# Kernel tuning notes

Measured on AMD Instinct MI355X. Metric: run time of the kernel, lower is better.

Reference implementation:

```python
import jax, jax.numpy as jnp
import numpy as np

NUM_HEADS = 16

def setup_inputs() -> dict:
    key = jax.random.key(0)
    k1, k2, k3 = jax.random.split(key, 3)
    B, N, D = 4, 2048, 1024
    init_attn_std = D ** (-0.5)
    x = jax.random.normal(k1, (B, N, D), dtype=jnp.float32)
    qkv_w = jax.random.normal(k2, (D, 3 * D), dtype=jnp.float32) * init_attn_std
    proj_w = jax.random.normal(k3, (D, D), dtype=jnp.float32) * init_attn_std
    proj_b = jnp.zeros((D,), dtype=jnp.float32)
    return {"x": x, "qkv_w": qkv_w, "proj_w": proj_w, "proj_b": proj_b}

def reference(x, qkv_w, proj_w, proj_b):
    B, N, D = x.shape
    H = NUM_HEADS
    hd = D // H
    scale = hd ** (-0.5)
    # QKV projection (no bias, qkv_bias=False)
    qkv = (x @ qkv_w).reshape(B, N, 3, H, hd)
    q, k, v = jnp.moveaxis(qkv, 2, 0)  # each [B, N, H, hd]
    # scaled dot-product attention with causal mask (matches flax nn.dot_product_attention)
    scores = jnp.einsum('bqhd,bkhd->bhqk', q * scale, k)  # [B, H, N, N]
    causal = jnp.tril(jnp.ones((N, N), dtype=bool))
    big_neg = jnp.finfo(scores.dtype).min
    scores = jnp.where(causal, scores, big_neg)
    attn = jax.nn.softmax(scores, axis=-1)
    out = jnp.einsum('bhqk,bkhd->bqhd', attn, v).reshape(B, N, D)
    # output projection (proj_bias=True)
    return out @ proj_w + proj_b
```

## Files before the change

### kernel.cpp

```cpp
#include <hip/hip_runtime.h>

typedef __attribute__((ext_vector_type(8))) short sh8;
typedef __attribute__((ext_vector_type(8))) __bf16 bf8v;
typedef __attribute__((ext_vector_type(4))) float f4v;
typedef __attribute__((ext_vector_type(16))) float f16v;
typedef __attribute__((ext_vector_type(4))) unsigned u4v;

__device__ __forceinline__ float fast_exp2(float x) { return __builtin_amdgcn_exp2f(x); }

__device__ __forceinline__ unsigned short f2bf(float f) {
  unsigned u = __builtin_bit_cast(unsigned, f);
  u += 0x7fffu + ((u >> 16) & 1u);
  return (unsigned short)(u >> 16);
}
__device__ __forceinline__ float bf2f(unsigned short h) {
  unsigned u = ((unsigned)h) << 16;
  return __builtin_bit_cast(float, u);
}

__device__ __forceinline__ void glds16(const unsigned short* g, unsigned short* l) {
  __builtin_amdgcn_global_load_lds((const __attribute__((address_space(1))) void*)g,
                                   (__attribute__((address_space(3))) void*)l, 16, 0, 0);
}

__global__ __launch_bounds__(256) void cast_kernel(const float* __restrict__ in,
                                                   unsigned short* __restrict__ out) {
  const int idx = (blockIdx.x * 256 + threadIdx.x) * 4;
  const float4 v = *(const float4*)(in + idx);
  ushort4 o;
  o.x = f2bf(v.x); o.y = f2bf(v.y); o.z = f2bf(v.z); o.w = f2bf(v.w);
  *(ushort4*)(out + idx) = o;
}

__global__ __launch_bounds__(256) void transpose_cast_kernel(const float* __restrict__ in,
                                                             unsigned short* __restrict__ out,
                                                             int R, int C) {
  __shared__ float tile[32][33];
  const int c0 = blockIdx.x * 32, r0 = blockIdx.y * 32;
  const int tx = threadIdx.x, ty = threadIdx.y;
#pragma unroll
  for (int i = 0; i < 4; ++i)
    tile[ty + 8 * i][tx] = in[(size_t)(r0 + ty + 8 * i) * C + c0 + tx];
  __syncthreads();
#pragma unroll
  for (int i = 0; i < 4; ++i)
    out[(size_t)(c0 + ty + 8 * i) * R + r0 + tx] = f2bf(tile[tx][ty + 8 * i]);
}

__global__ __launch_bounds__(256) void transpose_v_kernel(
    const unsigned short* __restrict__ V, unsigned short* __restrict__ Vt) {
  __shared__ alignas(16) unsigned short T[64 * 64];
  const int bh = blockIdx.y;
  const int n0 = blockIdx.x * 64;
  const int tid = threadIdx.x;
  {
    const int r = tid >> 2;
    const int seg = tid & 3;
#pragma unroll
    for (int s = 0; s < 2; ++s) {
      const int sg = seg + 4 * s;
      const sh8 v = *(const sh8*)&V[((size_t)bh * 2048 + n0 + r) * 64 + sg * 8];
      *(sh8*)&T[r * 64 + ((sg * 8) ^ ((r & 7) << 3))] = v;
    }
  }
  __syncthreads();
  const int d = tid & 63;
  const int h2 = tid >> 6;
  unsigned buf[8];
#pragma unroll
  for (int t = 0; t < 8; ++t) {
    const int n1 = h2 * 16 + 2 * t;
    const unsigned short a = T[n1 * 64 + (d ^ ((n1 & 7) << 3))];
    const unsigned short b = T[(n1 + 1) * 64 + (d ^ (((n1 + 1) & 7) << 3))];
    buf[t] = (unsigned)a | ((unsigned)b << 16);
  }
  unsigned short* dst = Vt + ((size_t)bh * 64 + d) * 2048 + n0 + h2 * 16;
  *(uint4*)dst = *(uint4*)&buf[0];
  *(uint4*)(dst + 8) = *(uint4*)&buf[4];
}

template <int MODE>
__global__ __launch_bounds__(256) void gemm_bf16_kernel(
    const unsigned short* __restrict__ A,
    const unsigned short* __restrict__ Bt,
    int M, int N, int K,
    unsigned short* __restrict__ q_out, unsigned short* __restrict__ k_out,
    unsigned short* __restrict__ v_out,
    const float* __restrict__ bias, float* __restrict__ c_out) {
  constexpr int BM = 128, BN = 128, BK = 32;
  __shared__ alignas(16) unsigned short As[BM * 32];
  __shared__ alignas(16) unsigned short Bs[BN * 32];
  const int tid = threadIdx.x;
  const int lane = tid & 63;
  const int wave = tid >> 6;
  const int wr = (wave >> 1) * 64;
  const int wc = (wave & 1) * 64;
  const int bm = blockIdx.x * BM;
  const int bn = blockIdx.y * BN;
  const int fr = lane & 15;
  const int kq = lane >> 4;

  f4v acc[4][4] = {};

  const int r16 = lane >> 2;
  const int slot = (lane & 3) ^ (r16 & 3);

  for (int k0 = 0; k0 < K; k0 += BK) {
    __syncthreads();
#pragma unroll
    for (int s = 0; s < 2; ++s) {
      const int rbase = wave * 32 + s * 16;
      glds16(&A[(size_t)(bm + rbase + r16) * K + k0 + slot * 8], &As[rbase * 32]);
      glds16(&Bt[(size_t)(bn + rbase + r16) * K + k0 + slot * 8], &Bs[rbase * 32]);
    }
    __syncthreads();
    bf8v af[4], bfv[4];
#pragma unroll
    for (int m = 0; m < 4; ++m) {
      const int row = wr + m * 16 + fr;
      af[m] = __builtin_bit_cast(bf8v, *(const sh8*)&As[row * 32 + ((kq * 8) ^ ((row & 3) << 3))]);
    }
#pragma unroll
    for (int n = 0; n < 4; ++n) {
      const int row = wc + n * 16 + fr;
      bfv[n] = __builtin_bit_cast(bf8v, *(const sh8*)&Bs[row * 32 + ((kq * 8) ^ ((row & 3) << 3))]);
    }
#pragma unroll
    for (int m = 0; m < 4; ++m)
#pragma unroll
      for (int n = 0; n < 4; ++n)
        acc[m][n] = __builtin_amdgcn_mfma_f32_16x16x32_bf16(af[m], bfv[n], acc[m][n], 0, 0, 0);
  }

#pragma unroll
  for (int m = 0; m < 4; ++m) {
#pragma unroll
    for (int n = 0; n < 4; ++n) {
#pragma unroll
      for (int i = 0; i < 4; ++i) {
        const int r = bm + wr + m * 16 + kq * 4 + i;
        const int c = bn + wc + n * 16 + fr;
        const float val = acc[m][n][i];
        if (MODE == 0) {
          const int b = r >> 11, nidx = r & 2047;
          const int which = c >> 10, rem = c & 1023;
          const int h = rem >> 6, d = rem & 63;
          const size_t off = ((size_t)((b * 16 + h) * 2048 + nidx)) * 64 + d;
          if (which == 0)      q_out[off] = f2bf(val * 0.18033688f);
          else if (which == 1) k_out[off] = f2bf(val);
          else                 v_out[off] = f2bf(val);
        } else {
          c_out[(size_t)r * N + c] = val + bias[c];
        }
      }
    }
  }
}

__global__ __launch_bounds__(256, 2) void attn_kernel(
    const unsigned short* __restrict__ Q, const unsigned short* __restrict__ Kg,
    const unsigned short* __restrict__ Vtg, unsigned short* __restrict__ O) {
  __shared__ alignas(16) unsigned short Ks[4][64 * 64];
  __shared__ alignas(16) unsigned short Vts[4][64 * 64];
  const int tid = threadIdx.x;
  const int lane = tid & 63;
  const int w = tid >> 6;
  const int q31 = lane & 31, hi = lane >> 5;
  const int sw = (lane & 7) << 3;
  const int wg = (blockIdx.x & 7) * 64 + (blockIdx.x >> 3);
  const int bh = wg >> 3;
  const int pair = wg & 7;
  const int qtA = pair, qtB = 15 - pair;
  const unsigned short* Qb = Q + (size_t)bh * (2048 * 64);
  const unsigned short* Kb = Kg + (size_t)bh * (2048 * 64);
  const unsigned short* Vtb = Vtg + (size_t)bh * (64 * 2048);
  const int q0wA = qtA * 128 + w * 32;
  const int q0wB = qtB * 128 + w * 32;

  bf8v qfA[4], qfB[4];
#pragma unroll
  for (int dk = 0; dk < 4; ++dk) {
    qfA[dk] = __builtin_bit_cast(bf8v, *(const sh8*)&Qb[(size_t)(q0wA + q31) * 64 + 8 * hi + 16 * dk]);
    qfB[dk] = __builtin_bit_cast(bf8v, *(const sh8*)&Qb[(size_t)(q0wB + q31) * 64 + 8 * hi + 16 * dk]);
  }

  f16v oA0 = {}, oA1 = {}, oB0 = {}, oB1 = {};
  float mA = -1e30f, lA = 0.f, mB = -1e30f, lB = 0.f;

  const int r8 = lane >> 3;
  const int gslot = (lane & 7) ^ r8;
  const int rb0 = w * 16, rb1 = w * 16 + 8;

#define STAGE(g)                                                                              \
  {                                                                                           \
    const int _b = (g) & 3;                                                                   \
    glds16(&Kb[(size_t)((g) * 64 + rb0 + r8) * 64 + gslot * 8], &Ks[_b][rb0 * 64]);           \
    glds16(&Kb[(size_t)((g) * 64 + rb1 + r8) * 64 + gslot * 8], &Ks[_b][rb1 * 64]);           \
    glds16(&Vtb[(size_t)(rb0 + r8) * 2048 + (g) * 64 + gslot * 8], &Vts[_b][rb0 * 64]);       \
    glds16(&Vtb[(size_t)(rb1 + r8) * 2048 + (g) * 64 + gslot * 8], &Vts[_b][rb1 * 64]);       \
  }

  auto body = [&](int j, int buf, int q0w, bf8v (&qf)[4], f16v& o0, f16v& o1,
                  float& m_i, float& l_i) {
    f16v s0 = {}, s1 = {};
    __builtin_amdgcn_s_setprio(1);
#pragma unroll
    for (int dk = 0; dk < 4; ++dk) {
      const int col = (8 * hi + 16 * dk) ^ sw;
      const bf8v k0 = __builtin_bit_cast(bf8v, *(const sh8*)&Ks[buf][q31 * 64 + col]);
      const bf8v k1 = __builtin_bit_cast(bf8v, *(const sh8*)&Ks[buf][(32 + q31) * 64 + col]);
      s0 = __builtin_amdgcn_mfma_f32_32x32x16_bf16(k0, qf[dk], s0, 0, 0, 0);
      s1 = __builtin_amdgcn_mfma_f32_32x32x16_bf16(k1, qf[dk], s1, 0, 0, 0);
    }
    __builtin_amdgcn_s_setprio(0);

    const int qg = q0w + q31;
    if (j * 64 + 63 > q0w) {
#pragma unroll
      for (int r = 0; r < 16; ++r) {
        const int kl = j * 64 + (r & 3) + 8 * (r >> 2) + 4 * hi;
        if (kl > qg) s0[r] = -1e30f;
        if (kl + 32 > qg) s1[r] = -1e30f;
      }
    }

    float mx = -1e30f;
#pragma unroll
    for (int r = 0; r < 16; ++r) mx = fmaxf(mx, fmaxf(s0[r], s1[r]));
    mx = fmaxf(mx, __shfl_xor(mx, 32));

    if (!__all(mx - m_i <= 8.f)) {
      const float mn = fmaxf(m_i, mx);
      const float alpha = fast_exp2(m_i - mn);
      m_i = mn;
      l_i *= alpha;
#pragma unroll
      for (int r = 0; r < 16; ++r) {
        const float ar = __shfl(alpha, (r & 3) + 8 * (r >> 2) + 4 * hi);
        o0[r] *= ar;
        o1[r] *= ar;
      }
    }

    float ps = 0.f;
#pragma unroll
    for (int r = 0; r < 16; ++r) {
      s0[r] = fast_exp2(s0[r] - m_i);
      s1[r] = fast_exp2(s1[r] - m_i);
      ps += s0[r] + s1[r];
    }
    ps += __shfl_xor(ps, 32);
    l_i += ps;

    unsigned w0[8], w1[8];
#pragma unroll
    for (int jj = 0; jj < 8; ++jj) {
      asm("v_cvt_pk_bf16_f32 %0, %1, %2" : "=v"(w0[jj]) : "v"(s0[2 * jj]), "v"(s0[2 * jj + 1]));
      asm("v_cvt_pk_bf16_f32 %0, %1, %2" : "=v"(w1[jj]) : "v"(s1[2 * jj]), "v"(s1[2 * jj + 1]));
    }

#pragma unroll
    for (int ks = 0; ks < 4; ++ks) {
      const int j0 = 4 * (ks & 1);
      unsigned x0 = (ks < 2 ? w0[j0 + 0] : w1[j0 + 0]);
      unsigned y0 = (ks < 2 ? w0[j0 + 2] : w1[j0 + 2]);
      unsigned x1 = (ks < 2 ? w0[j0 + 1] : w1[j0 + 1]);
      unsigned y1 = (ks < 2 ? w0[j0 + 3] : w1[j0 + 3]);
      asm("v_permlane32_swap_b32 %0, %1" : "+v"(x0), "+v"(y0));
      asm("v_permlane32_swap_b32 %0, %1" : "+v"(x1), "+v"(y1));
      u4v pw;
      pw[0] = x0; pw[1] = x1; pw[2] = y0; pw[3] = y1;
      const bf8v pa = __builtin_bit_cast(bf8v, pw);

      const int colv = (8 * hi + 16 * ks) ^ sw;
      const bf8v vf0 = __builtin_bit_cast(bf8v, *(const sh8*)&Vts[buf][q31 * 64 + colv]);
      const bf8v vf1 = __builtin_bit_cast(bf8v, *(const sh8*)&Vts[buf][(32 + q31) * 64 + colv]);
      __builtin_amdgcn_s_setprio(1);
      o0 = __builtin_amdgcn_mfma_f32_32x32x16_bf16(pa, vf0, o0, 0, 0, 0);
      o1 = __builtin_amdgcn_mfma_f32_32x32x16_bf16(pa, vf1, o1, 0, 0, 0);
      __builtin_amdgcn_s_setprio(0);
    }
  };

  const int b = bh >> 4, h = bh & 15;
  auto epi = [&](int q0w, f16v& o0, f16v& o1, float l_i) {
    const float rl = 1.f / l_i;
#pragma unroll
    for (int r = 0; r < 16; ++r) {
      const int cr = (r & 3) + 8 * (r >> 2) + 4 * hi;
      const float lr = __shfl(rl, cr);
      const size_t base = ((size_t)(b * 2048 + q0w + cr)) * 1024 + h * 64 + q31;
      O[base] = f2bf(o0[r] * lr);
      O[base + 32] = f2bf(o1[r] * lr);
    }
  };

  const int nA = 2 * qtA + 2;
  const int nT = 2 * qtB + 2;

  STAGE(0);
  STAGE(1);

  for (int j = 0; j < nT; ++j) {
    const int buf = j & 3;
    if (j + 2 < nT) {
      STAGE(j + 2);
      asm volatile("s_waitcnt vmcnt(8)" ::: "memory");
    } else if (j + 1 < nT) {
      asm volatile("s_waitcnt vmcnt(4)" ::: "memory");
    } else {
      asm volatile("s_waitcnt vmcnt(0)" ::: "memory");
    }
    __builtin_amdgcn_s_barrier();

    if (j < nA) body(j, buf, q0wA, qfA, oA0, oA1, mA, lA);
    body(j, buf, q0wB, qfB, oB0, oB1, mB, lB);

    if (j == nA - 1) epi(q0wA, oA0, oA1, lA);
  }
#undef STAGE

  epi(q0wB, oB0, oB1, lB);
}

extern "C" void kernel_launch(void* const* d_in, const int* in_sizes, int n_in,
                              void* d_out, int out_size, void* d_ws, size_t ws_size,
                              hipStream_t stream) {
  const float* x      = (const float*)d_in[0];
  const float* qkv_w  = (const float*)d_in[1];
  const float* proj_w = (const float*)d_in[2];
  const float* proj_b = (const float*)d_in[3];
  float* out = (float*)d_out;

  unsigned short* ws = (unsigned short*)d_ws;
  const size_t NE = (size_t)8192 * 1024;
  unsigned short* xb     = ws;
  unsigned short* wqkvT  = xb + NE;
  unsigned short* wprojT = wqkvT + (size_t)3072 * 1024;
  unsigned short* qb     = wprojT + (size_t)1024 * 1024;
  unsigned short* kb     = qb + NE;
  unsigned short* vb     = kb + NE;
  unsigned short* vt     = vb + NE;
  unsigned short* ab     = xb;

  cast_kernel<<<8192, 256, 0, stream>>>(x, xb);
  transpose_cast_kernel<<<dim3(96, 32), dim3(32, 8), 0, stream>>>(qkv_w, wqkvT, 1024, 3072);
  transpose_cast_kernel<<<dim3(32, 32), dim3(32, 8), 0, stream>>>(proj_w, wprojT, 1024, 1024);

  gemm_bf16_kernel<0><<<dim3(64, 24), 256, 0, stream>>>(
      xb, wqkvT, 8192, 3072, 1024, qb, kb, vb, nullptr, nullptr);

  transpose_v_kernel<<<dim3(32, 64), 256, 0, stream>>>(vb, vt);

  attn_kernel<<<512, 256, 0, stream>>>(qb, kb, vt, ab);

  gemm_bf16_kernel<1><<<dim3(64, 8), 256, 0, stream>>>(
      ab, wprojT, 8192, 1024, 1024, nullptr, nullptr, nullptr, proj_b, out);
}
```

Baseline: 194.1 us.

## Pipeline GEMM global-to-LDS loads with a 4-buffer, 2-ahead prefetch ring

Replaces the single-buffered GEMM K-loop, which synchronised twice per tile, with a 4-slot LDS ring. Loads are issued two tiles ahead and a single barrier per iteration is gated by explicit vmcnt waits. It also changes the LDS swizzle pattern, raises wave priority around the MFMA block, and requests 2 blocks per CU via launch bounds. The aim is to hide global load latency behind MFMA work, at the cost of 4x the LDS footprint and more register pressure.

```diff
diff --git a/kernel.cpp b/kernel.cpp
--- a/kernel.cpp
+++ b/kernel.cpp
@@ -80,57 +80,75 @@
 }
 
 template <int MODE>
-__global__ __launch_bounds__(256) void gemm_bf16_kernel(
+__global__ __launch_bounds__(256, 2) void gemm_bf16_kernel(
     const unsigned short* __restrict__ A,
     const unsigned short* __restrict__ Bt,
     int M, int N, int K,
     unsigned short* __restrict__ q_out, unsigned short* __restrict__ k_out,
     unsigned short* __restrict__ v_out,
     const float* __restrict__ bias, float* __restrict__ c_out) {
-  constexpr int BM = 128, BN = 128, BK = 32;
-  __shared__ alignas(16) unsigned short As[BM * 32];
-  __shared__ alignas(16) unsigned short Bs[BN * 32];
+  __shared__ alignas(16) unsigned short As[4 * 128 * 32];
+  __shared__ alignas(16) unsigned short Bs[4 * 128 * 32];
   const int tid = threadIdx.x;
   const int lane = tid & 63;
   const int wave = tid >> 6;
   const int wr = (wave >> 1) * 64;
   const int wc = (wave & 1) * 64;
-  const int bm = blockIdx.x * BM;
-  const int bn = blockIdx.y * BN;
+  const int bm = blockIdx.x * 128;
+  const int bn = blockIdx.y * 128;
   const int fr = lane & 15;
   const int kq = lane >> 4;
 
   f4v acc[4][4] = {};
 
   const int r16 = lane >> 2;
-  const int slot = (lane & 3) ^ (r16 & 3);
-
-  for (int k0 = 0; k0 < K; k0 += BK) {
-    __syncthreads();
-#pragma unroll
-    for (int s = 0; s < 2; ++s) {
-      const int rbase = wave * 32 + s * 16;
-      glds16(&A[(size_t)(bm + rbase + r16) * K + k0 + slot * 8], &As[rbase * 32]);
-      glds16(&Bt[(size_t)(bn + rbase + r16) * K + k0 + slot * 8], &Bs[rbase * 32]);
-    }
-    __syncthreads();
+  const int srcsl = (lane & 3) ^ ((r16 >> 1) & 3);
+  const int rb0 = wave * 32, rb1 = wave * 32 + 16;
+
+#define GSTAGE(g)                                                                            \
+  {                                                                                          \
+    const int _b = ((g) & 3) * 4096;                                                         \
+    const int _k0 = (g) * 32;                                                                \
+    glds16(&A[(size_t)(bm + rb0 + r16) * K + _k0 + srcsl * 8], &As[_b + rb0 * 32]);          \
+    glds16(&A[(size_t)(bm + rb1 + r16) * K + _k0 + srcsl * 8], &As[_b + rb1 * 32]);          \
+    glds16(&Bt[(size_t)(bn + rb0 + r16) * K + _k0 + srcsl * 8], &Bs[_b + rb0 * 32]);         \
+    glds16(&Bt[(size_t)(bn + rb1 + r16) * K + _k0 + srcsl * 8], &Bs[_b + rb1 * 32]);         \
+  }
+
+  const int nT = K >> 5;
+  GSTAGE(0);
+  GSTAGE(1);
+
+  const int rsl = (kq ^ ((fr >> 1) & 3)) * 8;
+
+  for (int j = 0; j < nT; ++j) {
+    const int buf = (j & 3) * 4096;
+    if (j + 2 < nT) {
+      GSTAGE(j + 2);
+      asm volatile("s_waitcnt vmcnt(8)" ::: "memory");
+    } else if (j + 1 < nT) {
+      asm volatile("s_waitcnt vmcnt(4)" ::: "memory");
+    } else {
+      asm volatile("s_waitcnt vmcnt(0)" ::: "memory");
+    }
+    __builtin_amdgcn_s_barrier();
+
     bf8v af[4], bfv[4];
 #pragma unroll
-    for (int m = 0; m < 4; ++m) {
-      const int row = wr + m * 16 + fr;
-      af[m] = __builtin_bit_cast(bf8v, *(const sh8*)&As[row * 32 + ((kq * 8) ^ ((row & 3) << 3))]);
-    }
-#pragma unroll
-    for (int n = 0; n < 4; ++n) {
-      const int row = wc + n * 16 + fr;
-      bfv[n] = __builtin_bit_cast(bf8v, *(const sh8*)&Bs[row * 32 + ((kq * 8) ^ ((row & 3) << 3))]);
-    }
+    for (int m = 0; m < 4; ++m)
+      af[m] = __builtin_bit_cast(bf8v, *(const sh8*)&As[buf + (wr + m * 16 + fr) * 32 + rsl]);
+#pragma unroll
+    for (int n = 0; n < 4; ++n)
+      bfv[n] = __builtin_bit_cast(bf8v, *(const sh8*)&Bs[buf + (wc + n * 16 + fr) * 32 + rsl]);
+    __builtin_amdgcn_s_setprio(1);
 #pragma unroll
     for (int m = 0; m < 4; ++m)
 #pragma unroll
       for (int n = 0; n < 4; ++n)
         acc[m][n] = __builtin_amdgcn_mfma_f32_16x16x32_bf16(af[m], bfv[n], acc[m][n], 0, 0, 0);
-  }
+    __builtin_amdgcn_s_setprio(0);
+  }
+#undef GSTAGE
 
 #pragma unroll
   for (int m = 0; m < 4; ++m) {
```

Measured after the change: 184.2 us. -5.1%, faster.
